# Kernel tuning notes

Hardware: AMD Instinct MI355X
Metric: run time of the kernel (lower is better)

## Reference

```python
import jax, jax.numpy as jnp
import numpy as np

MAX_NUM_NODES = 100000
HIDDEN_DIM = 128
EVENT_SEQ_LEN = 262144


def setup_inputs() -> dict:
    key = jax.random.key(0)
    ks = jax.random.split(key, 12)
    L, H, N = EVENT_SEQ_LEN, HIDDEN_DIM, MAX_NUM_NODES
    return {
        "event_type_ids": jax.random.randint(ks[0], (L,), 0, 10),
        "src_ids": jax.random.randint(ks[1], (L,), 0, N),
        "src_mask": jax.random.uniform(ks[2], (L,), dtype=jnp.float32),
        "dst_ids": jax.random.randint(ks[3], (L,), 0, N),
        "dst_mask": jax.random.uniform(ks[4], (L,), dtype=jnp.float32),
        "event_embeddings": jax.random.normal(ks[5], (L, H), dtype=jnp.float32),
        "event_mask": jax.random.uniform(ks[6], (L,), dtype=jnp.float32),
        "event_timestamps": jax.random.uniform(ks[7], (L,), dtype=jnp.float32) * 100.0,
        # learned / state parameters
        "memory": jax.random.normal(ks[8], (N, H), dtype=jnp.float32),
        "last_update": jax.random.uniform(ks[9], (N,), dtype=jnp.float32) * 100.0,
        "time_w": jax.random.normal(ks[10], (H,), dtype=jnp.float32),
        "time_b": jax.random.normal(ks[11], (H,), dtype=jnp.float32),
    }


def _time_encode(t, w, b):
    # TGN time encoder: cos(Linear(1 -> H)(t))
    return jnp.cos(t[:, None] * w[None, :] + b[None, :])


def _scatter_mean(messages, ids, num_segments):
    sums = jax.ops.segment_sum(messages, ids, num_segments=num_segments)
    counts = jax.ops.segment_sum(jnp.ones((messages.shape[0],), messages.dtype), ids,
                                 num_segments=num_segments)
    return sums / jnp.maximum(counts, 1.0)[:, None]


def reference(event_type_ids, src_ids, src_mask, dst_ids, dst_mask,
              event_embeddings, event_mask, event_timestamps,
              memory, last_update, time_w, time_b):
    H = memory.shape[1]
    L = event_type_ids.shape[0]
    # message()
    event_type_embs = jnp.broadcast_to(
        event_type_ids.astype(memory.dtype)[:, None], (L, H))
    src_embs = memory[src_ids] * src_mask[:, None]
    dst_embs = memory[dst_ids] * dst_mask[:, None]
    src_last_update = last_update[src_ids]
    dst_last_update = last_update[dst_ids]
    # NOTE: original code multiplies src_last_update by dst_mask (faithful copy)
    src_timestamp_emb = _time_encode(event_timestamps - src_last_update * dst_mask, time_w, time_b)
    dst_timestamp_emb = _time_encode(event_timestamps - dst_last_update * dst_mask, time_w, time_b)
    src_messages = jnp.concatenate(
        [event_type_embs, src_embs, dst_embs, src_timestamp_emb, event_embeddings],
        axis=1) * event_mask[:, None]
    dst_messages = jnp.concatenate(
        [event_type_embs, dst_embs, src_embs, dst_timestamp_emb, event_embeddings],
        axis=1) * dst_mask[:, None]
    # agg_message(): scatter-mean over node ids
    src_agg = _scatter_mean(src_messages, src_ids, MAX_NUM_NODES)
    dst_agg = _scatter_mean(dst_messages, dst_ids, MAX_NUM_NODES)
    return jnp.stack([src_agg, dst_agg])  # (2, max_num_nodes, 5*hidden_dim)
```

## Files before the change

kernel.cpp:

```cpp
#include <hip/hip_runtime.h>

#define NODES 100000
#define HD 128
#define MSG 640
#define NS (2 * NODES)


__global__ void tgn_count_kernel(const int* __restrict__ src_ids,
                                 const int* __restrict__ dst_ids,
                                 int* __restrict__ cnt, int L) {
    int i = blockIdx.x * blockDim.x + threadIdx.x;
    if (i < L) {
        atomicAdd(&cnt[src_ids[i]], 1);
        atomicAdd(&cnt[NODES + dst_ids[i]], 1);
    }
}

__global__ void tgn_alloc_kernel(const int* __restrict__ cnt,
                                 int* __restrict__ off,
                                 int* __restrict__ cursor,
                                 int* __restrict__ gcur, int n) {
    int i = blockIdx.x * blockDim.x + threadIdx.x;
    int lane = threadIdx.x & 63;
    int c = (i < n) ? cnt[i] : 0;
    int p = c;
    #pragma unroll
    for (int o = 1; o < 64; o <<= 1) {
        int t = __shfl_up(p, o);
        if (lane >= o) p += t;
    }
    int total = __shfl(p, 63);
    int base = 0;
    if (lane == 63) base = atomicAdd(gcur, total);
    base = __shfl(base, 63);
    if (i < n) {
        int o = base + p - c;
        off[i] = o;
        cursor[i] = o;
    }
}

__global__ void tgn_fill_kernel(const int* __restrict__ src_ids,
                                const int* __restrict__ dst_ids,
                                int* __restrict__ cursor,
                                int* __restrict__ list, int L) {
    int i = blockIdx.x * blockDim.x + threadIdx.x;
    if (i < L) {
        int ps = atomicAdd(&cursor[src_ids[i]], 1);
        list[ps] = i;
        int pd = atomicAdd(&cursor[NODES + dst_ids[i]], 1);
        list[pd] = i;
    }
}

__global__ __launch_bounds__(256) void tgn_node_kernel(
        const int* __restrict__ event_type_ids,
        const int* __restrict__ src_ids,
        const float* __restrict__ src_mask,
        const int* __restrict__ dst_ids,
        const float* __restrict__ dst_mask,
        const float* __restrict__ event_embeddings,
        const float* __restrict__ event_mask,
        const float* __restrict__ event_timestamps,
        const float* __restrict__ memory,
        const float* __restrict__ last_update,
        const float* __restrict__ time_w,
        const float* __restrict__ time_b,
        const int* __restrict__ cnt,
        const int* __restrict__ off,
        const int* __restrict__ list,
        float* __restrict__ out) {
    int wid = (int)((blockIdx.x * (long long)blockDim.x + threadIdx.x) >> 6);
    int lane = threadIdx.x & 63;
    if (wid >= NS) return;

    bool is_src = wid < NODES;
    int node = is_src ? wid : wid - NODES;
    int c = cnt[wid];
    int o = off[wid];

    float w0 = time_w[lane], w1 = time_w[lane + 64];
    float b0 = time_b[lane], b1 = time_b[lane + 64];
    float self_m0 = memory[(size_t)node * HD + lane];
    float self_m1 = memory[(size_t)node * HD + lane + 64];
    float lu_self = last_update[node];

    float a_typ = 0.f;
    float a_s0 = 0.f, a_s1 = 0.f;
    float a_o0 = 0.f, a_o1 = 0.f;
    float a_t0 = 0.f, a_t1 = 0.f;
    float a_e0 = 0.f, a_e1 = 0.f;

    for (int j = 0; j < c; ++j) {
        int e = list[o + j];
        int s = src_ids[e];
        int d = dst_ids[e];
        float sm = src_mask[e];
        float dm = dst_mask[e];
        float em = event_mask[e];
        float ts = event_timestamps[e];
        float typ = (float)event_type_ids[e];

        int other = is_src ? d : s;
        float scale = is_src ? em : dm;
        float self_mask = is_src ? sm : dm;
        float other_mask = is_src ? dm : sm;

        float om0 = memory[(size_t)other * HD + lane] * other_mask;
        float om1 = memory[(size_t)other * HD + lane + 64] * other_mask;
        float tphase = ts - lu_self * dm;
        float t0 = __cosf(tphase * w0 + b0);
        float t1 = __cosf(tphase * w1 + b1);
        float e0 = event_embeddings[(size_t)e * HD + lane];
        float e1 = event_embeddings[(size_t)e * HD + lane + 64];

        a_typ += typ * scale;
        a_s0 += self_m0 * self_mask * scale;
        a_s1 += self_m1 * self_mask * scale;
        a_o0 += om0 * scale;
        a_o1 += om1 * scale;
        a_t0 += t0 * scale;
        a_t1 += t1 * scale;
        a_e0 += e0 * scale;
        a_e1 += e1 * scale;
    }

    float inv = (c > 0) ? (1.0f / (float)c) : 0.0f;
    float* row = out + (size_t)wid * MSG;
    __builtin_nontemporal_store(a_typ * inv, row + 0 * HD + lane);
    __builtin_nontemporal_store(a_typ * inv, row + 0 * HD + lane + 64);
    __builtin_nontemporal_store(a_s0 * inv, row + 1 * HD + lane);
    __builtin_nontemporal_store(a_s1 * inv, row + 1 * HD + lane + 64);
    __builtin_nontemporal_store(a_o0 * inv, row + 2 * HD + lane);
    __builtin_nontemporal_store(a_o1 * inv, row + 2 * HD + lane + 64);
    __builtin_nontemporal_store(a_t0 * inv, row + 3 * HD + lane);
    __builtin_nontemporal_store(a_t1 * inv, row + 3 * HD + lane + 64);
    __builtin_nontemporal_store(a_e0 * inv, row + 4 * HD + lane);
    __builtin_nontemporal_store(a_e1 * inv, row + 4 * HD + lane + 64);
}

extern "C" void kernel_launch(void* const* d_in, const int* in_sizes, int n_in,
                              void* d_out, int out_size, void* d_ws, size_t ws_size,
                              hipStream_t stream) {
    const int* event_type_ids = (const int*)d_in[0];
    const int* src_ids = (const int*)d_in[1];
    const float* src_mask = (const float*)d_in[2];
    const int* dst_ids = (const int*)d_in[3];
    const float* dst_mask = (const float*)d_in[4];
    const float* event_embeddings = (const float*)d_in[5];
    const float* event_mask = (const float*)d_in[6];
    const float* event_timestamps = (const float*)d_in[7];
    const float* memory = (const float*)d_in[8];
    const float* last_update = (const float*)d_in[9];
    const float* time_w = (const float*)d_in[10];
    const float* time_b = (const float*)d_in[11];

    int L = in_sizes[0];
    float* out = (float*)d_out;

    int* cnt = (int*)d_ws;
    int* gcur = cnt + NS;
    int* off = gcur + 1;
    int* cursor = off + NS;
    int* list = cursor + NS;

    hipMemsetAsync(cnt, 0, (size_t)(NS + 1) * sizeof(int), stream);

    int threads = 256;
    tgn_count_kernel<<<(L + threads - 1) / threads, threads, 0, stream>>>(
        src_ids, dst_ids, cnt, L);

    tgn_alloc_kernel<<<(NS + threads - 1) / threads, threads, 0, stream>>>(
        cnt, off, cursor, gcur, NS);

    tgn_fill_kernel<<<(L + threads - 1) / threads, threads, 0, stream>>>(
        src_ids, dst_ids, cursor, list, L);

    long long total_threads = (long long)NS * 64;
    int blocks = (int)((total_threads + threads - 1) / threads);
    tgn_node_kernel<<<blocks, threads, 0, stream>>>(
        event_type_ids, src_ids, src_mask, dst_ids, dst_mask,
        event_embeddings, event_mask, event_timestamps,
        memory, last_update, time_w, time_b,
        cnt, off, list, out);
}
```

Before: 841.3 us.

## Pack per-event metadata into CSR records and vectorize node gather

The fill kernel now writes a 32-byte record per (node, event) entry holding the other node id, event index, masks, timestamp and type. The node kernel therefore reads one contiguous record instead of seven scattered per-event arrays. The node kernel also prefetches the next record, loads and stores float2 per lane with wave-uniform count and offset, and drops the is_src branching. The cost is a larger workspace and more writes in the fill kernel. Each lane now handles adjacent column pairs, which changes how memory rows map across lanes.

```diff
diff --git a/kernel.cpp b/kernel.cpp
--- a/kernel.cpp
+++ b/kernel.cpp
@@ -4,6 +4,9 @@
 #define HD 128
 #define MSG 640
 #define NS (2 * NODES)
+
+typedef float f32x2 __attribute__((ext_vector_type(2)));
+typedef float f32x4 __attribute__((ext_vector_type(4)));
 
 
 __global__ void tgn_count_kernel(const int* __restrict__ src_ids,
@@ -40,103 +43,113 @@
     }
 }
 
-__global__ void tgn_fill_kernel(const int* __restrict__ src_ids,
+__global__ void tgn_fill_kernel(const int* __restrict__ event_type_ids,
+                                const int* __restrict__ src_ids,
+                                const float* __restrict__ src_mask,
                                 const int* __restrict__ dst_ids,
+                                const float* __restrict__ dst_mask,
+                                const float* __restrict__ event_mask,
+                                const float* __restrict__ event_timestamps,
                                 int* __restrict__ cursor,
-                                int* __restrict__ list, int L) {
+                                f32x4* __restrict__ rec, int L) {
     int i = blockIdx.x * blockDim.x + threadIdx.x;
-    if (i < L) {
-        int ps = atomicAdd(&cursor[src_ids[i]], 1);
-        list[ps] = i;
-        int pd = atomicAdd(&cursor[NODES + dst_ids[i]], 1);
-        list[pd] = i;
-    }
+    if (i >= L) return;
+    int s = src_ids[i];
+    int d = dst_ids[i];
+    float sm = src_mask[i];
+    float dm = dst_mask[i];
+    float em = event_mask[i];
+    float ts = event_timestamps[i];
+    float typ = (float)event_type_ids[i];
+
+    int ps = atomicAdd(&cursor[s], 1);
+    rec[(size_t)ps * 2]     = (f32x4){__int_as_float(d), __int_as_float(i), em, sm};
+    rec[(size_t)ps * 2 + 1] = (f32x4){dm, dm, ts, typ};
+
+    int pd = atomicAdd(&cursor[NODES + d], 1);
+    rec[(size_t)pd * 2]     = (f32x4){__int_as_float(s), __int_as_float(i), dm, dm};
+    rec[(size_t)pd * 2 + 1] = (f32x4){sm, dm, ts, typ};
 }
 
 __global__ __launch_bounds__(256) void tgn_node_kernel(
-        const int* __restrict__ event_type_ids,
-        const int* __restrict__ src_ids,
-        const float* __restrict__ src_mask,
-        const int* __restrict__ dst_ids,
-        const float* __restrict__ dst_mask,
         const float* __restrict__ event_embeddings,
-        const float* __restrict__ event_mask,
-        const float* __restrict__ event_timestamps,
         const float* __restrict__ memory,
         const float* __restrict__ last_update,
         const float* __restrict__ time_w,
         const float* __restrict__ time_b,
         const int* __restrict__ cnt,
         const int* __restrict__ off,
-        const int* __restrict__ list,
+        const f32x4* __restrict__ rec,
         float* __restrict__ out) {
     int wid = (int)((blockIdx.x * (long long)blockDim.x + threadIdx.x) >> 6);
     int lane = threadIdx.x & 63;
     if (wid >= NS) return;
 
-    bool is_src = wid < NODES;
-    int node = is_src ? wid : wid - NODES;
-    int c = cnt[wid];
-    int o = off[wid];
+    int node = (wid < NODES) ? wid : (wid - NODES);
+    int c = __builtin_amdgcn_readfirstlane(cnt[wid]);
+    int o = __builtin_amdgcn_readfirstlane(off[wid]);
 
-    float w0 = time_w[lane], w1 = time_w[lane + 64];
-    float b0 = time_b[lane], b1 = time_b[lane + 64];
-    float self_m0 = memory[(size_t)node * HD + lane];
-    float self_m1 = memory[(size_t)node * HD + lane + 64];
-    float lu_self = last_update[node];
+    const f32x2* mem2 = (const f32x2*)memory;
+    const f32x2* emb2 = (const f32x2*)event_embeddings;
+    f32x2 wv = ((const f32x2*)time_w)[lane];
+    f32x2 bv = ((const f32x2*)time_b)[lane];
+    f32x2 selfm = mem2[(size_t)node * 64 + lane];
+    float lu = last_update[node];
 
     float a_typ = 0.f;
-    float a_s0 = 0.f, a_s1 = 0.f;
-    float a_o0 = 0.f, a_o1 = 0.f;
-    float a_t0 = 0.f, a_t1 = 0.f;
-    float a_e0 = 0.f, a_e1 = 0.f;
+    f32x2 a_s = {0.f, 0.f};
+    f32x2 a_o = {0.f, 0.f};
+    f32x2 a_t = {0.f, 0.f};
+    f32x2 a_e = {0.f, 0.f};
 
-    for (int j = 0; j < c; ++j) {
-        int e = list[o + j];
-        int s = src_ids[e];
-        int d = dst_ids[e];
-        float sm = src_mask[e];
-        float dm = dst_mask[e];
-        float em = event_mask[e];
-        float ts = event_timestamps[e];
-        float typ = (float)event_type_ids[e];
+    if (c > 0) {
+        f32x4 lo = rec[(size_t)o * 2];
+        f32x4 hi = rec[(size_t)o * 2 + 1];
+        for (int j = 0; j < c; ++j) {
+            f32x4 clo = lo, chi = hi;
+            int jn = (j + 1 < c) ? (j + 1) : j;
+            lo = rec[(size_t)(o + jn) * 2];
+            hi = rec[(size_t)(o + jn) * 2 + 1];
 
-        int other = is_src ? d : s;
-        float scale = is_src ? em : dm;
-        float self_mask = is_src ? sm : dm;
-        float other_mask = is_src ? dm : sm;
+            int other        = __float_as_int(clo.x);
+            int e            = __float_as_int(clo.y);
+            float scale      = clo.z;
+            float self_mask  = clo.w;
+            float other_mask = chi.x;
+            float dm         = chi.y;
+            float ts         = chi.z;
+            float typ        = chi.w;
 
-        float om0 = memory[(size_t)other * HD + lane] * other_mask;
-        float om1 = memory[(size_t)other * HD + lane + 64] * other_mask;
-        float tphase = ts - lu_self * dm;
-        float t0 = __cosf(tphase * w0 + b0);
-        float t1 = __cosf(tphase * w1 + b1);
-        float e0 = event_embeddings[(size_t)e * HD + lane];
-        float e1 = event_embeddings[(size_t)e * HD + lane + 64];
+            f32x2 mo = mem2[(size_t)other * 64 + lane];
+            f32x2 ee = emb2[(size_t)e * 64 + lane];
+            float tphase = ts - lu * dm;
+            float t0 = __cosf(tphase * wv.x + bv.x);
+            float t1 = __cosf(tphase * wv.y + bv.y);
 
-        a_typ += typ * scale;
-        a_s0 += self_m0 * self_mask * scale;
-        a_s1 += self_m1 * self_mask * scale;
-        a_o0 += om0 * scale;
-        a_o1 += om1 * scale;
-        a_t0 += t0 * scale;
-        a_t1 += t1 * scale;
-        a_e0 += e0 * scale;
-        a_e1 += e1 * scale;
+            a_typ += typ * scale;
+            a_s.x += selfm.x * self_mask * scale;
+            a_s.y += selfm.y * self_mask * scale;
+            a_o.x += (mo.x * other_mask) * scale;
+            a_o.y += (mo.y * other_mask) * scale;
+            a_t.x += t0 * scale;
+            a_t.y += t1 * scale;
+            a_e.x += ee.x * scale;
+            a_e.y += ee.y * scale;
+        }
     }
 
     float inv = (c > 0) ? (1.0f / (float)c) : 0.0f;
-    float* row = out + (size_t)wid * MSG;
-    __builtin_nontemporal_store(a_typ * inv, row + 0 * HD + lane);
-    __builtin_nontemporal_store(a_typ * inv, row + 0 * HD + lane + 64);
-    __builtin_nontemporal_store(a_s0 * inv, row + 1 * HD + lane);
-    __builtin_nontemporal_store(a_s1 * inv, row + 1 * HD + lane + 64);
-    __builtin_nontemporal_store(a_o0 * inv, row + 2 * HD + lane);
-    __builtin_nontemporal_store(a_o1 * inv, row + 2 * HD + lane + 64);
-    __builtin_nontemporal_store(a_t0 * inv, row + 3 * HD + lane);
-    __builtin_nontemporal_store(a_t1 * inv, row + 3 * HD + lane + 64);
-    __builtin_nontemporal_store(a_e0 * inv, row + 4 * HD + lane);
-    __builtin_nontemporal_store(a_e1 * inv, row + 4 * HD + lane + 64);
+    f32x2* row = (f32x2*)(out + (size_t)wid * MSG);
+    f32x2 v0 = {a_typ * inv, a_typ * inv};
+    f32x2 v1 = {a_s.x * inv, a_s.y * inv};
+    f32x2 v2 = {a_o.x * inv, a_o.y * inv};
+    f32x2 v3 = {a_t.x * inv, a_t.y * inv};
+    f32x2 v4 = {a_e.x * inv, a_e.y * inv};
+    __builtin_nontemporal_store(v0, row + 0 * 64 + lane);
+    __builtin_nontemporal_store(v1, row + 1 * 64 + lane);
+    __builtin_nontemporal_store(v2, row + 2 * 64 + lane);
+    __builtin_nontemporal_store(v3, row + 3 * 64 + lane);
+    __builtin_nontemporal_store(v4, row + 4 * 64 + lane);
 }
 
 extern "C" void kernel_launch(void* const* d_in, const int* in_sizes, int n_in,
@@ -162,9 +175,9 @@
     int* gcur = cnt + NS;
     int* off = gcur + 1;
     int* cursor = off + NS;
-    int* list = cursor + NS;
+    f32x4* rec = (f32x4*)((char*)d_ws + (size_t)(3 * NS + 8) * sizeof(int));
 
-    hipMemsetAsync(cnt, 0, (size_t)(NS + 1) * sizeof(int), stream);
+    (void)hipMemsetAsync(cnt, 0, (size_t)(NS + 1) * sizeof(int), stream);
 
     int threads = 256;
     tgn_count_kernel<<<(L + threads - 1) / threads, threads, 0, stream>>>(
@@ -174,13 +187,12 @@
         cnt, off, cursor, gcur, NS);
 
     tgn_fill_kernel<<<(L + threads - 1) / threads, threads, 0, stream>>>(
-        src_ids, dst_ids, cursor, list, L);
+        event_type_ids, src_ids, src_mask, dst_ids, dst_mask,
+        event_mask, event_timestamps, cursor, rec, L);
 
     long long total_threads = (long long)NS * 64;
     int blocks = (int)((total_threads + threads - 1) / threads);
     tgn_node_kernel<<<blocks, threads, 0, stream>>>(
-        event_type_ids, src_ids, src_mask, dst_ids, dst_mask,
-        event_embeddings, event_mask, event_timestamps,
-        memory, last_update, time_w, time_b,
-        cnt, off, list, out);
+        event_embeddings, memory, last_update, time_w, time_b,
+        cnt, off, rec, out);
 }
```

Measured after the change: 778.6 us. 7.5% less time.
